# Performance work log

Measured on AMD Instinct MI355X. Metric: run time of the kernel, lower is better.

## Reference

```python
import jax, jax.numpy as jnp
import numpy as np

N = 50000
E = 400000
IN_DIM = 256
HID = 64
HEADS = 8
OUT_DIM = 40
NEG_SLOPE = 0.2  # PyG GATConv leaky-relu slope


def gat_conv(x, src, dst, W, a_src, a_dst, bias, concat):
    """One PyG-style GATConv (eval mode, self-loops already appended).
    x: [N, in], W: [in, H*C], a_src/a_dst: [H, C], bias: [H*C] or [C]."""
    H, C = a_src.shape
    h = (x @ W).reshape(N, H, C)                       # [N, H, C]
    # per-node attention logits, gathered per edge
    e_src = (h * a_src[None]).sum(-1)                  # [N, H]
    e_dst = (h * a_dst[None]).sum(-1)                  # [N, H]
    alpha = jax.nn.leaky_relu(e_src[src] + e_dst[dst], NEG_SLOPE)  # [Etot, H]
    # segment softmax over incoming edges of each dst node
    amax = jax.ops.segment_max(alpha, dst, num_segments=N)         # [N, H]
    ex = jnp.exp(alpha - amax[dst])
    denom = jax.ops.segment_sum(ex, dst, num_segments=N)           # [N, H]
    coef = ex / denom[dst]                                         # [Etot, H]
    # weighted scatter-add of neighbor features
    msg = h[src] * coef[:, :, None]                                # [Etot, H, C]
    out = jax.ops.segment_sum(msg, dst, num_segments=N)            # [N, H, C]
    out = out.reshape(N, H * C) if concat else out.mean(axis=1)
    return out + bias


def setup_inputs() -> dict:
    key = jax.random.key(0)
    ks = jax.random.split(key, 10)
    x = jax.random.normal(ks[0], (N, IN_DIM), dtype=jnp.float32)
    edge_index = jax.random.randint(ks[1], (2, E), 0, N, dtype=jnp.int32)
    g1 = 1.0 / np.sqrt(IN_DIM)
    g2 = 1.0 / np.sqrt(HID * HEADS)
    W1 = jax.random.normal(ks[2], (IN_DIM, HEADS * HID), dtype=jnp.float32) * g1
    a_src1 = jax.random.normal(ks[3], (HEADS, HID), dtype=jnp.float32) * 0.1
    a_dst1 = jax.random.normal(ks[4], (HEADS, HID), dtype=jnp.float32) * 0.1
    b1 = jnp.zeros((HEADS * HID,), dtype=jnp.float32)
    W2 = jax.random.normal(ks[5], (HEADS * HID, OUT_DIM), dtype=jnp.float32) * g2
    a_src2 = jax.random.normal(ks[6], (1, OUT_DIM), dtype=jnp.float32) * 0.1
    a_dst2 = jax.random.normal(ks[7], (1, OUT_DIM), dtype=jnp.float32) * 0.1
    b2 = jnp.zeros((OUT_DIM,), dtype=jnp.float32)
    return {"x": x, "edge_index": edge_index, "W1": W1, "a_src1": a_src1,
            "a_dst1": a_dst1, "b1": b1, "W2": W2, "a_src2": a_src2,
            "a_dst2": a_dst2, "b2": b2}


def reference(x, edge_index, W1, a_src1, a_dst1, b1, W2, a_src2, a_dst2, b2):
    # append self loops (PyG GATConv default add_self_loops=True)
    loop = jnp.arange(N, dtype=edge_index.dtype)
    src = jnp.concatenate([edge_index[0], loop])
    dst = jnp.concatenate([edge_index[1], loop])
    h = gat_conv(x, src, dst, W1, a_src1, a_dst1, b1, concat=True)
    h = jax.nn.elu(h)
    # dropout is identity in eval mode
    out = gat_conv(h, src, dst, W2, a_src2, a_dst2, b2, concat=False)
    return out
```

## Files before the change

### kernel.cpp

```cpp
#include <hip/hip_runtime.h>
#include <hip/hip_bf16.h>
#include <math.h>

#define IN_DIM 256
#define HEADS 8
#define HID 64
#define HC1 512
#define OUT_DIM 40
#define NEG_SLOPE 0.2f

typedef __attribute__((ext_vector_type(8))) short short8;
typedef __attribute__((ext_vector_type(4))) float f32x4;

__device__ __forceinline__ unsigned short f2b(float f) {
    __hip_bfloat16 h = __float2bfloat16(f);
    unsigned short u;
    __builtin_memcpy(&u, &h, 2);
    return u;
}


__global__ __launch_bounds__(256) void prep_w1t(
    const float* __restrict__ W1, __hip_bfloat16* __restrict__ W1T)
{
    int i = blockIdx.x * 256 + threadIdx.x;
    if (i >= HC1 * IN_DIM) return;
    int n = i >> 8, k = i & 255;
    W1T[i] = __float2bfloat16(W1[(size_t)k * HC1 + n]);
}

__global__ __launch_bounds__(256) void prep_w2t(
    const float* __restrict__ W2, __hip_bfloat16* __restrict__ W2T)
{
    int i = blockIdx.x * 256 + threadIdx.x;
    if (i >= 48 * HC1) return;
    int n = i >> 9, k = i & 511;
    W2T[i] = __float2bfloat16(n < OUT_DIM ? W2[(size_t)k * OUT_DIM + n] : 0.f);
}


__global__ __launch_bounds__(256) void degree_kernel(
    const int* __restrict__ ei, int* __restrict__ deg, int E, int ET)
{
    int e = blockIdx.x * 256 + threadIdx.x;
    if (e >= ET) return;
    int d = (e < E) ? ei[E + e] : e - E;
    atomicAdd(&deg[d], 1);
}

__global__ __launch_bounds__(256) void scan1_kernel(
    const int* __restrict__ deg, int* __restrict__ rowptr,
    int* __restrict__ aux, int N)
{
    __shared__ int sd[256];
    int tid = threadIdx.x;
    int i = blockIdx.x * 256 + tid;
    int v = (i < N) ? deg[i] : 0;
    sd[tid] = v;
    __syncthreads();
    for (int off = 1; off < 256; off <<= 1) {
        int t = (tid >= off) ? sd[tid - off] : 0;
        __syncthreads();
        sd[tid] += t;
        __syncthreads();
    }
    if (i < N) rowptr[i] = sd[tid] - v;
    if (tid == 255) aux[blockIdx.x] = sd[255];
}

__global__ __launch_bounds__(256) void scan_aux_kernel(int* __restrict__ aux, int nb)
{
    __shared__ int sd[256];
    int tid = threadIdx.x;
    int v = (tid < nb) ? aux[tid] : 0;
    sd[tid] = v;
    __syncthreads();
    for (int off = 1; off < 256; off <<= 1) {
        int t = (tid >= off) ? sd[tid - off] : 0;
        __syncthreads();
        sd[tid] += t;
        __syncthreads();
    }
    if (tid < nb) aux[tid] = sd[tid] - v;
}

__global__ __launch_bounds__(256) void scan_add_kernel(
    int* __restrict__ rowptr, const int* __restrict__ aux, int N, int ET)
{
    int i = blockIdx.x * 256 + threadIdx.x;
    if (i < N) rowptr[i] += aux[blockIdx.x];
    if (i == 0) rowptr[N] = ET;
}

__global__ __launch_bounds__(256) void build_kernel(
    const int* __restrict__ ei, int* __restrict__ cursor,
    int* __restrict__ csr_src, int E, int ET)
{
    int e = blockIdx.x * 256 + threadIdx.x;
    if (e >= ET) return;
    int s, d;
    if (e < E) { s = ei[e]; d = ei[E + e]; } else { s = d = e - E; }
    int pos = atomicAdd(&cursor[d], 1);
    csr_src[pos] = s;
}

__global__ __launch_bounds__(512) void gemm1_mfma(
    const float* __restrict__ x, const __hip_bfloat16* __restrict__ W1T,
    const float* __restrict__ a_src1, const float* __restrict__ a_dst1,
    __hip_bfloat16* __restrict__ h1, float* __restrict__ e_src1,
    float* __restrict__ e_dst1, int N)
{
    __shared__ __hip_bfloat16 As[64][264];
    const int tid = threadIdx.x;
    const int row0 = blockIdx.x * 64;

    {
        int rr = tid >> 3;
        int cb = (tid & 7) * 32;
        int rowc = row0 + rr; if (rowc >= N) rowc = N - 1;
        const float* xp = x + (size_t)rowc * IN_DIM + cb;
#pragma unroll
        for (int j = 0; j < 4; ++j) {
            float4 a0 = *(const float4*)(xp + 8 * j);
            float4 a1 = *(const float4*)(xp + 8 * j + 4);
            short8 v;
            v[0] = f2b(a0.x); v[1] = f2b(a0.y); v[2] = f2b(a0.z); v[3] = f2b(a0.w);
            v[4] = f2b(a1.x); v[5] = f2b(a1.y); v[6] = f2b(a1.z); v[7] = f2b(a1.w);
            *(short8*)(&As[rr][cb + 8 * j]) = v;
        }
    }
    __syncthreads();

    const int w = tid >> 6;
    const int lane = tid & 63;
    const int r = lane & 15, g = lane >> 4;

    f32x4 acc[4][4] = {};
    const short* bp = (const short*)W1T + (size_t)(w * 64 + r) * IN_DIM + 8 * g;

#pragma unroll 2
    for (int kk = 0; kk < IN_DIM; kk += 32) {
        short8 af[4];
#pragma unroll
        for (int rt = 0; rt < 4; ++rt)
            af[rt] = *(const short8*)(&As[rt * 16 + r][kk + 8 * g]);
        short8 bf[4];
#pragma unroll
        for (int t = 0; t < 4; ++t)
            bf[t] = *(const short8*)(bp + (size_t)t * 16 * IN_DIM + kk);
#pragma unroll
        for (int t = 0; t < 4; ++t)
#pragma unroll
            for (int rt = 0; rt < 4; ++rt)
                acc[rt][t] = __builtin_amdgcn_mfma_f32_16x16x32_bf16(
                    af[rt], bf[t], acc[rt][t], 0, 0, 0);
    }

#pragma unroll
    for (int rt = 0; rt < 4; ++rt)
#pragma unroll
        for (int t = 0; t < 4; ++t) {
            int c = w * 64 + t * 16 + r;
#pragma unroll
            for (int q = 0; q < 4; ++q) {
                int row = row0 + rt * 16 + 4 * g + q;
                if (row < N)
                    h1[(size_t)row * HC1 + c] = __float2bfloat16(acc[rt][t][q]);
            }
        }

    float a1v[4], a2v[4];
#pragma unroll
    for (int t = 0; t < 4; ++t) {
        a1v[t] = a_src1[w * 64 + t * 16 + r];
        a2v[t] = a_dst1[w * 64 + t * 16 + r];
    }
#pragma unroll
    for (int rt = 0; rt < 4; ++rt) {
        float ps[4] = {}, pd[4] = {};
#pragma unroll
        for (int t = 0; t < 4; ++t)
#pragma unroll
            for (int q = 0; q < 4; ++q) {
                ps[q] += acc[rt][t][q] * a1v[t];
                pd[q] += acc[rt][t][q] * a2v[t];
            }
#pragma unroll
        for (int off = 1; off < 16; off <<= 1)
#pragma unroll
            for (int q = 0; q < 4; ++q) {
                ps[q] += __shfl_xor(ps[q], off);
                pd[q] += __shfl_xor(pd[q], off);
            }
        if (r == 0) {
#pragma unroll
            for (int q = 0; q < 4; ++q) {
                int row = row0 + rt * 16 + 4 * g + q;
                if (row < N) {
                    e_src1[row * 8 + w] = ps[q];
                    e_dst1[row * 8 + w] = pd[q];
                }
            }
        }
    }
}

__global__ __launch_bounds__(256) void gather1_kernel(
    const int* __restrict__ rowptr, const int* __restrict__ csr_src,
    const __hip_bfloat16* __restrict__ h1, const float* __restrict__ e_src,
    const float* __restrict__ e_dst, const float* __restrict__ b1,
    __hip_bfloat16* __restrict__ hmid, int N)
{
    int d = blockIdx.x * 2 + (threadIdx.x >> 7);
    if (d >= N) return;
    int t = threadIdx.x & 127;
    int h0 = t >> 4;
    int base = rowptr[d], end = rowptr[d + 1];
    float ed = e_dst[d * 8 + h0];

    float a0f = 0.f, a1f = 0.f, a2f = 0.f, a3f = 0.f, ssum = 0.f;

#define LRELU(a) ((a) > 0.f ? (a) : NEG_SLOPE * (a))
#define ACCUM(u, e)                                          \
    {                                                        \
        a0f += (e) * __uint_as_float((u).x << 16);           \
        a1f += (e) * __uint_as_float((u).x & 0xffff0000u);   \
        a2f += (e) * __uint_as_float((u).y << 16);           \
        a3f += (e) * __uint_as_float((u).y & 0xffff0000u);   \
        ssum += (e);                                         \
    }

    int j = base;
    for (; j + 4 <= end; j += 4) {
        int s0 = csr_src[j], s1 = csr_src[j + 1], s2 = csr_src[j + 2], s3 = csr_src[j + 3];
        float v0 = e_src[s0 * 8 + h0] + ed;
        float v1 = e_src[s1 * 8 + h0] + ed;
        float v2 = e_src[s2 * 8 + h0] + ed;
        float v3 = e_src[s3 * 8 + h0] + ed;
        uint2 u0 = *(const uint2*)(h1 + (size_t)s0 * HC1 + 4 * t);
        uint2 u1 = *(const uint2*)(h1 + (size_t)s1 * HC1 + 4 * t);
        uint2 u2 = *(const uint2*)(h1 + (size_t)s2 * HC1 + 4 * t);
        uint2 u3 = *(const uint2*)(h1 + (size_t)s3 * HC1 + 4 * t);
        float e0 = __expf(LRELU(v0));
        float e1 = __expf(LRELU(v1));
        float e2 = __expf(LRELU(v2));
        float e3 = __expf(LRELU(v3));
        ACCUM(u0, e0); ACCUM(u1, e1); ACCUM(u2, e2); ACCUM(u3, e3);
    }
    for (; j < end; ++j) {
        int s0 = csr_src[j];
        float v0 = e_src[s0 * 8 + h0] + ed;
        uint2 u0 = *(const uint2*)(h1 + (size_t)s0 * HC1 + 4 * t);
        float e0 = __expf(LRELU(v0));
        ACCUM(u0, e0);
    }

    float inv = 1.f / ssum;
    const float4 bv = *(const float4*)(b1 + 4 * t);
    float o0 = a0f * inv + bv.x;
    float o1 = a1f * inv + bv.y;
    float o2 = a2f * inv + bv.z;
    float o3 = a3f * inv + bv.w;
    o0 = o0 > 0.f ? o0 : expm1f(o0);
    o1 = o1 > 0.f ? o1 : expm1f(o1);
    o2 = o2 > 0.f ? o2 : expm1f(o2);
    o3 = o3 > 0.f ? o3 : expm1f(o3);
    unsigned short rr[4] = { f2b(o0), f2b(o1), f2b(o2), f2b(o3) };
    *(uint2*)(hmid + (size_t)d * HC1 + 4 * t) = *(uint2*)rr;
}

__global__ __launch_bounds__(256) void gemm2_mfma(
    const __hip_bfloat16* __restrict__ hmid, const __hip_bfloat16* __restrict__ W2T,
    const float* __restrict__ a_src2, const float* __restrict__ a_dst2,
    float* __restrict__ h2, float* __restrict__ e_src2, float* __restrict__ e_dst2,
    int N)
{
    __shared__ __hip_bfloat16 Bs[48][520];
    const int tid = threadIdx.x;

    {
        const short* wp = (const short*)W2T;
#pragma unroll
        for (int i = 0; i < 12; ++i) {
            int idx = tid + i * 256;
            int row = idx >> 6, ch = idx & 63;
            *(short8*)(&Bs[row][ch * 8]) = *(const short8*)(wp + (size_t)row * HC1 + ch * 8);
        }
    }
    __syncthreads();

    const int w = tid >> 6;
    const int lane = tid & 63;
    const int r = lane & 15, g = lane >> 4;
    const int rowW = blockIdx.x * 64 + w * 16;

    int arow = rowW + r; if (arow >= N) arow = N - 1;
    const short* ap = (const short*)hmid + (size_t)arow * HC1 + 8 * g;

    f32x4 acc[3] = {};
#pragma unroll 4
    for (int kk = 0; kk < HC1; kk += 32) {
        short8 af = *(const short8*)(ap + kk);
        short8 bf[3];
#pragma unroll
        for (int t = 0; t < 3; ++t)
            bf[t] = *(const short8*)(&Bs[t * 16 + r][kk + 8 * g]);
#pragma unroll
        for (int t = 0; t < 3; ++t)
            acc[t] = __builtin_amdgcn_mfma_f32_16x16x32_bf16(af, bf[t], acc[t], 0, 0, 0);
    }

#pragma unroll
    for (int t = 0; t < 3; ++t) {
        int c = t * 16 + r;
        if (c < OUT_DIM) {
#pragma unroll
            for (int q = 0; q < 4; ++q) {
                int row = rowW + 4 * g + q;
                if (row < N) h2[(size_t)row * OUT_DIM + c] = acc[t][q];
            }
        }
    }

    float as[3], ad[3];
#pragma unroll
    for (int t = 0; t < 3; ++t) {
        int c = t * 16 + r;
        as[t] = (c < OUT_DIM) ? a_src2[c] : 0.f;
        ad[t] = (c < OUT_DIM) ? a_dst2[c] : 0.f;
    }
    float ps[4] = {}, pd[4] = {};
#pragma unroll
    for (int t = 0; t < 3; ++t)
#pragma unroll
        for (int q = 0; q < 4; ++q) {
            ps[q] += acc[t][q] * as[t];
            pd[q] += acc[t][q] * ad[t];
        }
#pragma unroll
    for (int off = 1; off < 16; off <<= 1)
#pragma unroll
        for (int q = 0; q < 4; ++q) {
            ps[q] += __shfl_xor(ps[q], off);
            pd[q] += __shfl_xor(pd[q], off);
        }
    if (r == 0) {
#pragma unroll
        for (int q = 0; q < 4; ++q) {
            int row = rowW + 4 * g + q;
            if (row < N) { e_src2[row] = ps[q]; e_dst2[row] = pd[q]; }
        }
    }
}

__global__ __launch_bounds__(256) void gather2_kernel(
    const int* __restrict__ rowptr, const int* __restrict__ csr_src,
    const float* __restrict__ h2, const float* __restrict__ e_src,
    const float* __restrict__ e_dst, const float* __restrict__ b2,
    float* __restrict__ out, int N)
{
    int wid = (blockIdx.x * blockDim.x + threadIdx.x) >> 6;
    if (wid >= N) return;
    int lane = threadIdx.x & 63;
    int base = rowptr[wid], end = rowptr[wid + 1];
    float ed = e_dst[wid];
    bool act = lane < OUT_DIM;
    int ln = act ? lane : 0;

    float acc = 0.f, ssum = 0.f;
    int j = base;
    for (; j + 4 <= end; j += 4) {
        int s0 = csr_src[j], s1 = csr_src[j + 1], s2 = csr_src[j + 2], s3 = csr_src[j + 3];
        float v0 = e_src[s0] + ed, v1 = e_src[s1] + ed;
        float v2 = e_src[s2] + ed, v3 = e_src[s3] + ed;
        float f0 = h2[(size_t)s0 * OUT_DIM + ln];
        float f1 = h2[(size_t)s1 * OUT_DIM + ln];
        float f2 = h2[(size_t)s2 * OUT_DIM + ln];
        float f3 = h2[(size_t)s3 * OUT_DIM + ln];
        float e0 = __expf(LRELU(v0)), e1 = __expf(LRELU(v1));
        float e2 = __expf(LRELU(v2)), e3 = __expf(LRELU(v3));
        acc += e0 * f0 + e1 * f1 + e2 * f2 + e3 * f3;
        ssum += e0 + e1 + e2 + e3;
    }
    for (; j < end; ++j) {
        int s0 = csr_src[j];
        float v0 = e_src[s0] + ed;
        float f0 = h2[(size_t)s0 * OUT_DIM + ln];
        float e0 = __expf(LRELU(v0));
        acc += e0 * f0;
        ssum += e0;
    }
    if (act)
        out[(size_t)wid * OUT_DIM + lane] = acc / ssum + b2[lane];
}

extern "C" void kernel_launch(void* const* d_in, const int* in_sizes, int n_in,
                              void* d_out, int out_size, void* d_ws, size_t ws_size,
                              hipStream_t stream)
{
    const float* x      = (const float*)d_in[0];
    const int*   ei     = (const int*)d_in[1];
    const float* W1     = (const float*)d_in[2];
    const float* a_src1 = (const float*)d_in[3];
    const float* a_dst1 = (const float*)d_in[4];
    const float* b1     = (const float*)d_in[5];
    const float* W2     = (const float*)d_in[6];
    const float* a_src2 = (const float*)d_in[7];
    const float* a_dst2 = (const float*)d_in[8];
    const float* b2     = (const float*)d_in[9];
    float* out = (float*)d_out;

    const int N  = in_sizes[0] / IN_DIM;
    const int E  = in_sizes[1] / 2;
    const int ET = E + N;

    char* p = (char*)d_ws;
    auto alloc = [&](size_t bytes) -> void* {
        void* r = (void*)p;
        p += (bytes + 255) & ~(size_t)255;
        return r;
    };
    __hip_bfloat16* h1b    = (__hip_bfloat16*)alloc((size_t)N * HC1 * 2);
    __hip_bfloat16* hmid   = (__hip_bfloat16*)alloc((size_t)N * HC1 * 2);
    float*    h2      = (float*)alloc((size_t)N * OUT_DIM * 4);
    float*    e_src1  = (float*)alloc((size_t)N * HEADS * 4);
    float*    e_dst1  = (float*)alloc((size_t)N * HEADS * 4);
    float*    e_src2  = (float*)alloc((size_t)N * 4);
    float*    e_dst2  = (float*)alloc((size_t)N * 4);
    int*      deg     = (int*)alloc((size_t)N * 4);
    int*      rowptr  = (int*)alloc((size_t)(N + 1) * 4);
    int*      cursor  = (int*)alloc((size_t)N * 4);
    int*      csr_src = (int*)alloc((size_t)ET * 4);
    int*      aux     = (int*)alloc(256 * 4);
    __hip_bfloat16* W1T = (__hip_bfloat16*)alloc((size_t)HC1 * IN_DIM * 2);
    __hip_bfloat16* W2T = (__hip_bfloat16*)alloc((size_t)48 * HC1 * 2);

    const int nbN  = (N + 255) / 256;
    const int nbET = (ET + 255) / 256;

    prep_w1t<<<(HC1 * IN_DIM + 255) / 256, 256, 0, stream>>>(W1, W1T);
    prep_w2t<<<(48 * HC1 + 255) / 256, 256, 0, stream>>>(W2, W2T);

    hipMemsetAsync(deg, 0, (size_t)N * 4, stream);
    degree_kernel<<<nbET, 256, 0, stream>>>(ei, deg, E, ET);
    scan1_kernel<<<nbN, 256, 0, stream>>>(deg, rowptr, aux, N);
    scan_aux_kernel<<<1, 256, 0, stream>>>(aux, nbN);
    scan_add_kernel<<<nbN, 256, 0, stream>>>(rowptr, aux, N, ET);
    hipMemcpyAsync(cursor, rowptr, (size_t)N * 4, hipMemcpyDeviceToDevice, stream);
    build_kernel<<<nbET, 256, 0, stream>>>(ei, cursor, csr_src, E, ET);

    gemm1_mfma<<<(N + 63) / 64, 512, 0, stream>>>(x, W1T, a_src1, a_dst1, h1b,
                                                  e_src1, e_dst1, N);
    gather1_kernel<<<(N + 1) / 2, 256, 0, stream>>>(rowptr, csr_src, h1b, e_src1,
                                                    e_dst1, b1, hmid, N);

    gemm2_mfma<<<(N + 63) / 64, 256, 0, stream>>>(hmid, W2T, a_src2, a_dst2, h2,
                                                  e_src2, e_dst2, N);
    gather2_kernel<<<(N + 3) / 4, 256, 0, stream>>>(rowptr, csr_src, h2, e_src2,
                                                    e_dst2, b2, out, N);
}
```

Before: 240.8 us.

## Use one wave per node with shuffled edge coefficients in GAT gathers

Measured after the change: 246.9 us. 2.5% more time.

```diff
diff --git a/kernel.cpp b/kernel.cpp
--- a/kernel.cpp
+++ b/kernel.cpp
@@ -19,23 +19,22 @@
     return u;
 }
 
-
-__global__ __launch_bounds__(256) void prep_w1t(
-    const float* __restrict__ W1, __hip_bfloat16* __restrict__ W1T)
+#define LRELU(a) ((a) > 0.f ? (a) : NEG_SLOPE * (a))
+
+__global__ __launch_bounds__(256) void prep_weights(
+    const float* __restrict__ W1, const float* __restrict__ W2,
+    __hip_bfloat16* __restrict__ W1T, __hip_bfloat16* __restrict__ W2T)
 {
     int i = blockIdx.x * 256 + threadIdx.x;
-    if (i >= HC1 * IN_DIM) return;
-    int n = i >> 8, k = i & 255;
-    W1T[i] = __float2bfloat16(W1[(size_t)k * HC1 + n]);
-}
-
-__global__ __launch_bounds__(256) void prep_w2t(
-    const float* __restrict__ W2, __hip_bfloat16* __restrict__ W2T)
-{
-    int i = blockIdx.x * 256 + threadIdx.x;
-    if (i >= 48 * HC1) return;
-    int n = i >> 9, k = i & 511;
-    W2T[i] = __float2bfloat16(n < OUT_DIM ? W2[(size_t)k * OUT_DIM + n] : 0.f);
+    if (i < HC1 * IN_DIM) {
+        int n = i >> 8, k = i & 255;
+        W1T[i] = __float2bfloat16(W1[(size_t)k * HC1 + n]);
+    }
+    int j = i - HC1 * IN_DIM;
+    if (j >= 0 && j < 48 * HC1) {
+        int n = j >> 9, k = j & 511;
+        W2T[j] = __float2bfloat16(n < OUT_DIM ? W2[(size_t)k * OUT_DIM + n] : 0.f);
+    }
 }
 
 
@@ -211,62 +210,58 @@
     const float* __restrict__ e_dst, const float* __restrict__ b1,
     __hip_bfloat16* __restrict__ hmid, int N)
 {
-    int d = blockIdx.x * 2 + (threadIdx.x >> 7);
+    int d = blockIdx.x * 4 + (threadIdx.x >> 6);
     if (d >= N) return;
-    int t = threadIdx.x & 127;
-    int h0 = t >> 4;
-    int base = rowptr[d], end = rowptr[d + 1];
-    float ed = e_dst[d * 8 + h0];
-
-    float a0f = 0.f, a1f = 0.f, a2f = 0.f, a3f = 0.f, ssum = 0.f;
-
-#define LRELU(a) ((a) > 0.f ? (a) : NEG_SLOPE * (a))
-#define ACCUM(u, e)                                          \
-    {                                                        \
-        a0f += (e) * __uint_as_float((u).x << 16);           \
-        a1f += (e) * __uint_as_float((u).x & 0xffff0000u);   \
-        a2f += (e) * __uint_as_float((u).y << 16);           \
-        a3f += (e) * __uint_as_float((u).y & 0xffff0000u);   \
-        ssum += (e);                                         \
-    }
-
-    int j = base;
-    for (; j + 4 <= end; j += 4) {
-        int s0 = csr_src[j], s1 = csr_src[j + 1], s2 = csr_src[j + 2], s3 = csr_src[j + 3];
-        float v0 = e_src[s0 * 8 + h0] + ed;
-        float v1 = e_src[s1 * 8 + h0] + ed;
-        float v2 = e_src[s2 * 8 + h0] + ed;
-        float v3 = e_src[s3 * 8 + h0] + ed;
-        uint2 u0 = *(const uint2*)(h1 + (size_t)s0 * HC1 + 4 * t);
-        uint2 u1 = *(const uint2*)(h1 + (size_t)s1 * HC1 + 4 * t);
-        uint2 u2 = *(const uint2*)(h1 + (size_t)s2 * HC1 + 4 * t);
-        uint2 u3 = *(const uint2*)(h1 + (size_t)s3 * HC1 + 4 * t);
-        float e0 = __expf(LRELU(v0));
-        float e1 = __expf(LRELU(v1));
-        float e2 = __expf(LRELU(v2));
-        float e3 = __expf(LRELU(v3));
-        ACCUM(u0, e0); ACCUM(u1, e1); ACCUM(u2, e2); ACCUM(u3, e3);
-    }
-    for (; j < end; ++j) {
-        int s0 = csr_src[j];
-        float v0 = e_src[s0 * 8 + h0] + ed;
-        uint2 u0 = *(const uint2*)(h1 + (size_t)s0 * HC1 + 4 * t);
-        float e0 = __expf(LRELU(v0));
-        ACCUM(u0, e0);
+    const int lane = threadIdx.x & 63;
+    const int h0 = lane >> 3;
+    const int base = rowptr[d];
+    const int deg = rowptr[d + 1] - base;
+    const float edv = e_dst[d * 8 + (lane & 7)];
+
+    float acc[8] = {};
+    float ssum = 0.f;
+
+    const int nch = (deg + 7) >> 3;
+    for (int c = 0; c < nch; ++c) {
+        int i = c * 8 + (lane >> 3);
+        int ii = i < deg ? i : deg - 1;
+        int s = csr_src[base + ii];
+        float v = e_src[s * 8 + (lane & 7)] + edv;
+        float coef = (i < deg) ? __expf(LRELU(v)) : 0.f;
+
+        int emax = deg - c * 8; if (emax > 8) emax = 8;
+        for (int e = 0; e < emax; ++e) {
+            float ce = __shfl(coef, e * 8 + h0);
+            int se = __shfl(s, e * 8);
+            uint4 u = *(const uint4*)(h1 + (size_t)se * HC1 + 8 * lane);
+            acc[0] += ce * __uint_as_float(u.x << 16);
+            acc[1] += ce * __uint_as_float(u.x & 0xffff0000u);
+            acc[2] += ce * __uint_as_float(u.y << 16);
+            acc[3] += ce * __uint_as_float(u.y & 0xffff0000u);
+            acc[4] += ce * __uint_as_float(u.z << 16);
+            acc[5] += ce * __uint_as_float(u.z & 0xffff0000u);
+            acc[6] += ce * __uint_as_float(u.w << 16);
+            acc[7] += ce * __uint_as_float(u.w & 0xffff0000u);
+            ssum += ce;
+        }
     }
 
     float inv = 1.f / ssum;
-    const float4 bv = *(const float4*)(b1 + 4 * t);
-    float o0 = a0f * inv + bv.x;
-    float o1 = a1f * inv + bv.y;
-    float o2 = a2f * inv + bv.z;
-    float o3 = a3f * inv + bv.w;
-    o0 = o0 > 0.f ? o0 : expm1f(o0);
-    o1 = o1 > 0.f ? o1 : expm1f(o1);
-    o2 = o2 > 0.f ? o2 : expm1f(o2);
-    o3 = o3 > 0.f ? o3 : expm1f(o3);
-    unsigned short rr[4] = { f2b(o0), f2b(o1), f2b(o2), f2b(o3) };
-    *(uint2*)(hmid + (size_t)d * HC1 + 4 * t) = *(uint2*)rr;
+    float4 b0 = *(const float4*)(b1 + 8 * lane);
+    float4 b4 = *(const float4*)(b1 + 8 * lane + 4);
+    float ob[8];
+    ob[0] = acc[0] * inv + b0.x; ob[1] = acc[1] * inv + b0.y;
+    ob[2] = acc[2] * inv + b0.z; ob[3] = acc[3] * inv + b0.w;
+    ob[4] = acc[4] * inv + b4.x; ob[5] = acc[5] * inv + b4.y;
+    ob[6] = acc[6] * inv + b4.z; ob[7] = acc[7] * inv + b4.w;
+    unsigned short rr[8];
+#pragma unroll
+    for (int j = 0; j < 8; ++j) {
+        float o = ob[j];
+        o = o > 0.f ? o : expm1f(o);
+        rr[j] = f2b(o);
+    }
+    *(uint4*)(hmid + (size_t)d * HC1 + 8 * lane) = *(uint4*)rr;
 }
 
 __global__ __launch_bounds__(256) void gemm2_mfma(
@@ -361,34 +356,30 @@
 {
     int wid = (blockIdx.x * blockDim.x + threadIdx.x) >> 6;
     if (wid >= N) return;
-    int lane = threadIdx.x & 63;
-    int base = rowptr[wid], end = rowptr[wid + 1];
-    float ed = e_dst[wid];
-    bool act = lane < OUT_DIM;
-    int ln = act ? lane : 0;
+    const int lane = threadIdx.x & 63;
+    const int base = rowptr[wid];
+    const int deg = rowptr[wid + 1] - base;
+    const float edv = e_dst[wid];
+    const bool act = lane < OUT_DIM;
 
     float acc = 0.f, ssum = 0.f;
-    int j = base;
-    for (; j + 4 <= end; j += 4) {
-        int s0 = csr_src[j], s1 = csr_src[j + 1], s2 = csr_src[j + 2], s3 = csr_src[j + 3];
-        float v0 = e_src[s0] + ed, v1 = e_src[s1] + ed;
-        float v2 = e_src[s2] + ed, v3 = e_src[s3] + ed;
-        float f0 = h2[(size_t)s0 * OUT_DIM + ln];
-        float f1 = h2[(size_t)s1 * OUT_DIM + ln];
-        float f2 = h2[(size_t)s2 * OUT_DIM + ln];
-        float f3 = h2[(size_t)s3 * OUT_DIM + ln];
-        float e0 = __expf(LRELU(v0)), e1 = __expf(LRELU(v1));
-        float e2 = __expf(LRELU(v2)), e3 = __expf(LRELU(v3));
-        acc += e0 * f0 + e1 * f1 + e2 * f2 + e3 * f3;
-        ssum += e0 + e1 + e2 + e3;
-    }
-    for (; j < end; ++j) {
-        int s0 = csr_src[j];
-        float v0 = e_src[s0] + ed;
-        float f0 = h2[(size_t)s0 * OUT_DIM + ln];
-        float e0 = __expf(LRELU(v0));
-        acc += e0 * f0;
-        ssum += e0;
+    for (int c = 0; c < deg; c += 64) {
+        int i = c + lane;
+        int ii = i < deg ? i : deg - 1;
+        int s = csr_src[base + ii];
+        float v = e_src[s] + edv;
+        float coef = (i < deg) ? __expf(LRELU(v)) : 0.f;
+
+        int emax = deg - c; if (emax > 64) emax = 64;
+#pragma unroll 4
+        for (int e = 0; e < emax; ++e) {
+            float ce = __shfl(coef, e);
+            int se = __shfl(s, e);
+            if (act) {
+                acc += ce * h2[(size_t)se * OUT_DIM + lane];
+                ssum += ce;
+            }
+        }
     }
     if (act)
         out[(size_t)wid * OUT_DIM + lane] = acc / ssum + b2[lane];
@@ -438,8 +429,8 @@
     const int nbN  = (N + 255) / 256;
     const int nbET = (ET + 255) / 256;
 
-    prep_w1t<<<(HC1 * IN_DIM + 255) / 256, 256, 0, stream>>>(W1, W1T);
-    prep_w2t<<<(48 * HC1 + 255) / 256, 256, 0, stream>>>(W2, W2T);
+    prep_weights<<<(HC1 * IN_DIM + 48 * HC1 + 255) / 256, 256, 0, stream>>>(
+        W1, W2, W1T, W2T);
 
     hipMemsetAsync(deg, 0, (size_t)N * 4, stream);
     degree_kernel<<<nbET, 256, 0, stream>>>(ei, deg, E, ET);
@@ -451,7 +442,7 @@
 
     gemm1_mfma<<<(N + 63) / 64, 512, 0, stream>>>(x, W1T, a_src1, a_dst1, h1b,
                                                   e_src1, e_dst1, N);
-    gather1_kernel<<<(N + 1) / 2, 256, 0, stream>>>(rowptr, csr_src, h1b, e_src1,
+    gather1_kernel<<<(N + 3) / 4, 256, 0, stream>>>(rowptr, csr_src, h1b, e_src1,
                                                     e_dst1, b1, hmid, N);
 
     gemm2_mfma<<<(N + 63) / 64, 256, 0, stream>>>(hmid, W2T, a_src2, a_dst2, h2,
```
